# Kernel tuning notes

Measured on AMD Instinct MI355X. Metric: run time of the kernel, lower is better.

## Reference

```python
import jax, jax.numpy as jnp
import numpy as np

T, D, H, E, TOP_K = 4096, 512, 2048, 16, 2


def setup_inputs() -> dict:
    key = jax.random.key(0)
    ks = jax.random.split(key, 4)
    x = jax.random.normal(ks[0], (T, D), dtype=jnp.float32)
    Wg = jax.random.normal(ks[1], (D, E), dtype=jnp.float32) * 0.02
    bg = jnp.zeros((E,), dtype=jnp.float32)
    W1 = jax.random.normal(ks[2], (E, D, H), dtype=jnp.float32) * 0.02
    b1 = jnp.zeros((E, H), dtype=jnp.float32)
    W2 = jax.random.normal(ks[3], (E, H, D), dtype=jnp.float32) * 0.02
    b2 = jnp.zeros((E, D), dtype=jnp.float32)
    return {"x": x, "Wg": Wg, "bg": bg, "W1": W1, "b1": b1, "W2": W2, "b2": b2}


def reference(x, Wg, bg, W1, b1, W2, b2):
    # NaiveGate: linear -> top-k -> softmax over the k selected logits
    logits = x @ Wg + bg                               # [T, E]
    gate_vals, gate_idx = jax.lax.top_k(logits, TOP_K)  # [T, k]
    gate_score = jax.nn.softmax(gate_vals, axis=-1)     # returned by gate; NOT applied to output (faithful to source)

    # combine weights: how many top-k slots of each token map to each expert
    counts = jax.nn.one_hot(gate_idx, E, dtype=x.dtype).sum(axis=1)  # [T, E]

    # Expert FFN (grouped GEMM expressed densely over the fixed expert axis)
    h = jax.nn.gelu(jnp.einsum('td,edh->eth', x, W1) + b1[:, None, :])  # [E, T, H]
    y = jnp.einsum('eth,ehd->etd', h, W2) + b2[:, None, :]              # [E, T, D]

    # Combine: unweighted sum over the token's top-k experts (matches .sum(dim=1) in source)
    out = jnp.einsum('etd,te->td', y, counts)                            # [T, D]
    return out, gate_idx, gate_score
```

## Files before the change

### kernel.cpp

```cpp
#include <hip/hip_runtime.h>
#include <math.h>

#define T_ 4096
#define D_ 512
#define H_ 2048
#define E_ 16
#define RCAP 10240

typedef short bf16x8 __attribute__((ext_vector_type(8)));
typedef float f32x4 __attribute__((ext_vector_type(4)));

__device__ __forceinline__ unsigned short f2bf(float f) {
  union { float f; unsigned u; } v; v.f = f;
  unsigned r = v.u + 0x7fffu + ((v.u >> 16) & 1u);
  return (unsigned short)(r >> 16);
}
__device__ __forceinline__ float bf2f(unsigned short u) {
  union { unsigned u; float f; } v; v.u = ((unsigned)u) << 16;
  return v.f;
}

__global__ void gate_kernel(const float* __restrict__ x,
                            const float* __restrict__ Wg,
                            const float* __restrict__ bg,
                            float* __restrict__ out,
                            int* __restrict__ tok2e) {
  const int lane = threadIdx.x & 63;
  const int t = blockIdx.x * 4 + (threadIdx.x >> 6);
  const int e = lane & 15, q = lane >> 4;
  const float4* x4 = (const float4*)(x + (size_t)t * D_ + q * 128);
  float acc = 0.f;
#pragma unroll 4
  for (int i = 0; i < 32; ++i) {
    float4 v = x4[i];
    const float* wp = Wg + (q * 128 + i * 4) * E_ + e;
    acc += v.x * wp[0];
    acc += v.y * wp[E_];
    acc += v.z * wp[2 * E_];
    acc += v.w * wp[3 * E_];
  }
  acc += __shfl_xor(acc, 16);
  acc += __shfl_xor(acc, 32);
  const float logit = acc + bg[e];
  float v1 = logit; int i1 = e;
#pragma unroll
  for (int s = 1; s < 16; s <<= 1) {
    float ov = __shfl_xor(v1, s); int oi = __shfl_xor(i1, s);
    if (ov > v1 || (ov == v1 && oi < i1)) { v1 = ov; i1 = oi; }
  }
  float v2 = (e == i1) ? -INFINITY : logit; int i2 = e;
#pragma unroll
  for (int s = 1; s < 16; s <<= 1) {
    float ov = __shfl_xor(v2, s); int oi = __shfl_xor(i2, s);
    if (ov > v2 || (ov == v2 && oi < i2)) { v2 = ov; i2 = oi; }
  }
  if (lane == 0) {
    const float ed = __expf(v2 - v1);
    const float inv = 1.f / (1.f + ed);
    const size_t gidx = (size_t)T_ * D_;
    out[gidx + t * 2]     = (float)i1;
    out[gidx + t * 2 + 1] = (float)i2;
    out[gidx + T_ * 2 + t * 2]     = inv;
    out[gidx + T_ * 2 + t * 2 + 1] = ed * inv;
    tok2e[t * 2] = i1; tok2e[t * 2 + 1] = i2;
  }
}

__global__ void count_kernel(const int* __restrict__ tok2e,
                             int* __restrict__ cnt2,
                             int* __restrict__ offs, int* __restrict__ tileoff,
                             int* __restrict__ rowbuf) {
  __shared__ int h[E_];
  if (threadIdx.x < E_) h[threadIdx.x] = 0;
  __syncthreads();
  for (int i = threadIdx.x; i < 2 * T_; i += 256) atomicAdd(&h[tok2e[i]], 1);
  __syncthreads();
  if (threadIdx.x == 0) {
    int o = 0, to = 0;
    offs[0] = 0; tileoff[0] = 0;
    for (int e = 0; e < E_; ++e) {
      int mt = (h[e] + 127) >> 7;
      o += mt << 7; to += mt;
      offs[e + 1] = o; tileoff[e + 1] = to;
    }
  }
  for (int i = threadIdx.x; i < E_ * 16; i += 256) cnt2[i] = 0;
  for (int i = threadIdx.x; i < RCAP; i += 256) rowbuf[i] = -1;
}

__global__ void scatter_kernel(const int* __restrict__ tok2e, int* __restrict__ cnt2,
                               const int* __restrict__ offs, int* __restrict__ rowbuf,
                               int* __restrict__ tok2row) {
  const int t = blockIdx.x * blockDim.x + threadIdx.x;
#pragma unroll
  for (int k = 0; k < 2; ++k) {
    int e = tok2e[t * 2 + k];
    int slot = atomicAdd(&cnt2[e * 16], 1);
    int row = offs[e] + slot;
    rowbuf[row] = t;
    tok2row[t * 2 + k] = row;
  }
}

__global__ void gather_kernel(const float* __restrict__ x,
                              const int* __restrict__ rowbuf,
                              const int* __restrict__ offs,
                              unsigned short* __restrict__ xg) {
  const int row = blockIdx.x;
  if (row >= offs[16]) return;
  const int t = rowbuf[row];
  const int lane = threadIdx.x;
  float4 a = make_float4(0.f, 0.f, 0.f, 0.f), b = a;
  if (t >= 0) {
    const float4* p = (const float4*)(x + (size_t)t * D_ + lane * 8);
    a = p[0]; b = p[1];
  }
  unsigned w0 = f2bf(a.x) | (f2bf(a.y) << 16);
  unsigned w1 = f2bf(a.z) | (f2bf(a.w) << 16);
  unsigned w2 = f2bf(b.x) | (f2bf(b.y) << 16);
  unsigned w3 = f2bf(b.z) | (f2bf(b.w) << 16);
  *(uint4*)(xg + (size_t)row * D_ + lane * 8) = make_uint4(w0, w1, w2, w3);
}

template <int KDIM, int NTOT, bool GELU>
__global__ __launch_bounds__(256) void ffn_gemm(
    const unsigned short* __restrict__ A_g, const float* __restrict__ B_g,
    const float* __restrict__ bias_g, unsigned short* __restrict__ out_g,
    const int* __restrict__ offs, const int* __restrict__ tileoff) {
  __shared__ unsigned short As[128][72];
  __shared__ unsigned short Bs[128][72];
  const int mt = blockIdx.x;
  if (mt >= tileoff[16]) return;
  int e = 0;
  while (tileoff[e + 1] <= mt) ++e;
  const int row0 = offs[e] + ((mt - tileoff[e]) << 7);
  const int n0 = blockIdx.y << 7;
  const int tid = threadIdx.x;
  const int lane = tid & 63;
  const int m_off = ((tid >> 6) & 1) << 6;
  const int n_off = (tid >> 7) << 6;

  f32x4 zero = {0.f, 0.f, 0.f, 0.f};
  f32x4 acc[4][4];
#pragma unroll
  for (int i = 0; i < 4; ++i)
#pragma unroll
    for (int j = 0; j < 4; ++j) acc[i][j] = zero;

  const int arow = tid >> 1, ahalf = tid & 1;
  const unsigned short* Aptr = A_g + (size_t)(row0 + arow) * KDIM + ahalf * 32;
  const int bn = tid & 127, bkq = tid >> 7;
  const float* Bptr = B_g + (size_t)e * KDIM * NTOT + (size_t)(bkq * 32) * NTOT + n0 + bn;

  for (int k0 = 0; k0 < KDIM; k0 += 64) {
    const uint4* asrc = (const uint4*)(Aptr + k0);
    uint4 a0 = asrc[0], a1 = asrc[1], a2 = asrc[2], a3 = asrc[3];
    const float* bsrc = Bptr + (size_t)k0 * NTOT;
    unsigned w[16];
#pragma unroll
    for (int kk = 0; kk < 16; ++kk) {
      unsigned lo = f2bf(bsrc[(size_t)(2 * kk) * NTOT]);
      unsigned hi = f2bf(bsrc[(size_t)(2 * kk + 1) * NTOT]);
      w[kk] = lo | (hi << 16);
    }
    uint4* adst = (uint4*)&As[arow][ahalf * 32];
    adst[0] = a0; adst[1] = a1; adst[2] = a2; adst[3] = a3;
    uint4* bdst = (uint4*)&Bs[bn][bkq * 32];
    bdst[0] = make_uint4(w[0], w[1], w[2], w[3]);
    bdst[1] = make_uint4(w[4], w[5], w[6], w[7]);
    bdst[2] = make_uint4(w[8], w[9], w[10], w[11]);
    bdst[3] = make_uint4(w[12], w[13], w[14], w[15]);
    __syncthreads();
#pragma unroll
    for (int kk = 0; kk < 64; kk += 32) {
      const int kidx = kk + ((lane >> 4) << 3);
      bf16x8 af[4], bfr[4];
#pragma unroll
      for (int i = 0; i < 4; ++i)
        af[i] = *(const bf16x8*)&As[m_off + i * 16 + (lane & 15)][kidx];
#pragma unroll
      for (int j = 0; j < 4; ++j)
        bfr[j] = *(const bf16x8*)&Bs[n_off + j * 16 + (lane & 15)][kidx];
#pragma unroll
      for (int i = 0; i < 4; ++i)
#pragma unroll
        for (int j = 0; j < 4; ++j)
          acc[i][j] = __builtin_amdgcn_mfma_f32_16x16x32_bf16(af[i], bfr[j], acc[i][j], 0, 0, 0);
    }
    __syncthreads();
  }
  const float* bias = bias_g + (size_t)e * NTOT;
  const int quad = lane >> 4, lcol = lane & 15;
#pragma unroll
  for (int j = 0; j < 4; ++j) {
    const int col = n0 + n_off + j * 16 + lcol;
    const float bv = bias[col];
#pragma unroll
    for (int i = 0; i < 4; ++i) {
      const int rbase = row0 + m_off + i * 16 + (quad << 2);
      f32x4 v = acc[i][j];
#pragma unroll
      for (int r = 0; r < 4; ++r) {
        float y = v[r] + bv;
        if (GELU) y = 0.5f * y * (1.f + erff(y * 0.70710678118f));
        out_g[(size_t)(rbase + r) * NTOT + col] = f2bf(y);
      }
    }
  }
}

__global__ void combine_kernel(const unsigned short* __restrict__ ybuf,
                               const int* __restrict__ tok2row,
                               float* __restrict__ out) {
  const int t = blockIdx.x, lane = threadIdx.x;
  const int rA = tok2row[t * 2], rB = tok2row[t * 2 + 1];
  const uint4 va = *(const uint4*)(ybuf + (size_t)rA * D_ + lane * 8);
  const uint4 vb = *(const uint4*)(ybuf + (size_t)rB * D_ + lane * 8);
  const unsigned short* pa = (const unsigned short*)&va;
  const unsigned short* pb = (const unsigned short*)&vb;
  float o[8];
#pragma unroll
  for (int i = 0; i < 8; ++i) o[i] = bf2f(pa[i]) + bf2f(pb[i]);
  float4* po = (float4*)(out + (size_t)t * D_ + lane * 8);
  po[0] = make_float4(o[0], o[1], o[2], o[3]);
  po[1] = make_float4(o[4], o[5], o[6], o[7]);
}

extern "C" void kernel_launch(void* const* d_in, const int* in_sizes, int n_in,
                              void* d_out, int out_size, void* d_ws, size_t ws_size,
                              hipStream_t stream) {
  const float* x  = (const float*)d_in[0];
  const float* Wg = (const float*)d_in[1];
  const float* bg = (const float*)d_in[2];
  const float* W1 = (const float*)d_in[3];
  const float* b1 = (const float*)d_in[4];
  const float* W2 = (const float*)d_in[5];
  const float* b2 = (const float*)d_in[6];
  float* out = (float*)d_out;
  char* ws = (char*)d_ws;

  int* cnt2    = (int*)(ws);
  int* offs    = (int*)(ws + 2048);
  int* tileoff = (int*)(ws + 3072);
  int* tok2e   = (int*)(ws + 4096);
  int* tok2row = (int*)(ws + 4096 + 32768);
  int* rowbuf  = (int*)(ws + 4096 + 65536);
  unsigned short* xg   = (unsigned short*)(ws + (1 << 20));
  unsigned short* ybuf = xg;
  unsigned short* hbuf = (unsigned short*)(ws + (12 << 20));

  gate_kernel<<<T_ / 4, 256, 0, stream>>>(x, Wg, bg, out, tok2e);
  count_kernel<<<1, 256, 0, stream>>>(tok2e, cnt2, offs, tileoff, rowbuf);
  scatter_kernel<<<T_ / 256, 256, 0, stream>>>(tok2e, cnt2, offs, rowbuf, tok2row);
  gather_kernel<<<RCAP, 64, 0, stream>>>(x, rowbuf, offs, xg);
  ffn_gemm<512, 2048, true><<<dim3(80, 16), 256, 0, stream>>>(xg, W1, b1, hbuf, offs, tileoff);
  ffn_gemm<2048, 512, false><<<dim3(80, 4), 256, 0, stream>>>(hbuf, W2, b2, ybuf, offs, tileoff);
  combine_kernel<<<T_, 64, 0, stream>>>(ybuf, tok2row, out);
}
```

Before: 341.7 us.

## Pre-transpose expert weights to bf16 K-major and shrink second GEMM N-tile

Adds a transpose kernel that converts each expert weight matrix from fp32 [K,N] to bf16 [N,K] before each GEMM. The GEMM then loads B tiles with contiguous 16-byte vector loads instead of strided scalar fp32 loads followed by in-loop conversion. The second GEMM also moves to a 64-wide N tile, which doubles its grid in y to expose more parallelism. The cost is an extra pass over the weights on every call, about 64MB of fp32 read and 32MB of bf16 written per matrix, plus more workspace.

```diff
diff --git a/kernel.cpp b/kernel.cpp
--- a/kernel.cpp
+++ b/kernel.cpp
@@ -122,69 +122,92 @@
   *(uint4*)(xg + (size_t)row * D_ + lane * 8) = make_uint4(w0, w1, w2, w3);
 }
 
-template <int KDIM, int NTOT, bool GELU>
+template <int K, int N>
+__global__ __launch_bounds__(256) void wtrans_kernel(const float* __restrict__ src,
+                                                     unsigned short* __restrict__ dst) {
+  __shared__ unsigned short tile[64][72];
+  const int e = blockIdx.z;
+  const int n0 = blockIdx.x << 6, k0 = blockIdx.y << 6;
+  const int tid = threadIdx.x;
+  const int tr = tid >> 4, tc = (tid & 15) << 2;
+  const float* s = src + ((size_t)e * K + k0) * N + n0;
+#pragma unroll
+  for (int p = 0; p < 4; ++p) {
+    float4 v = *(const float4*)(s + (size_t)(tr + p * 16) * N + tc);
+    tile[tc + 0][tr + p * 16] = f2bf(v.x);
+    tile[tc + 1][tr + p * 16] = f2bf(v.y);
+    tile[tc + 2][tr + p * 16] = f2bf(v.z);
+    tile[tc + 3][tr + p * 16] = f2bf(v.w);
+  }
+  __syncthreads();
+  const int wr = tid >> 2, wc = (tid & 3) << 4;
+  unsigned short* d = dst + ((size_t)e * N + n0 + wr) * K + k0 + wc;
+  *(uint4*)d       = *(const uint4*)&tile[wr][wc];
+  *(uint4*)(d + 8) = *(const uint4*)&tile[wr][wc + 8];
+}
+
+template <int KDIM, int NTOT, int NTILE, bool GELU>
 __global__ __launch_bounds__(256) void ffn_gemm(
-    const unsigned short* __restrict__ A_g, const float* __restrict__ B_g,
+    const unsigned short* __restrict__ A_g, const unsigned short* __restrict__ Bt_g,
     const float* __restrict__ bias_g, unsigned short* __restrict__ out_g,
     const int* __restrict__ offs, const int* __restrict__ tileoff) {
+  constexpr int JN = NTILE / 32;
   __shared__ unsigned short As[128][72];
-  __shared__ unsigned short Bs[128][72];
+  __shared__ unsigned short Bs[NTILE][72];
   const int mt = blockIdx.x;
   if (mt >= tileoff[16]) return;
   int e = 0;
   while (tileoff[e + 1] <= mt) ++e;
   const int row0 = offs[e] + ((mt - tileoff[e]) << 7);
-  const int n0 = blockIdx.y << 7;
+  const int n0 = blockIdx.y * NTILE;
   const int tid = threadIdx.x;
   const int lane = tid & 63;
   const int m_off = ((tid >> 6) & 1) << 6;
-  const int n_off = (tid >> 7) << 6;
-
-  f32x4 zero = {0.f, 0.f, 0.f, 0.f};
-  f32x4 acc[4][4];
+  const int n_off = (tid >> 7) * (NTILE / 2);
+
+  f32x4 acc[4][JN];
 #pragma unroll
   for (int i = 0; i < 4; ++i)
 #pragma unroll
-    for (int j = 0; j < 4; ++j) acc[i][j] = zero;
+    for (int j = 0; j < JN; ++j) acc[i][j] = (f32x4){0.f, 0.f, 0.f, 0.f};
 
   const int arow = tid >> 1, ahalf = tid & 1;
   const unsigned short* Aptr = A_g + (size_t)(row0 + arow) * KDIM + ahalf * 32;
-  const int bn = tid & 127, bkq = tid >> 7;
-  const float* Bptr = B_g + (size_t)e * KDIM * NTOT + (size_t)(bkq * 32) * NTOT + n0 + bn;
+  int brow, bcol;
+  if (NTILE == 128) { brow = tid >> 1; bcol = (tid & 1) * 32; }
+  else              { brow = tid >> 2; bcol = (tid & 3) * 16; }
+  const unsigned short* Bptr = Bt_g + ((size_t)e * NTOT + n0 + brow) * KDIM + bcol;
 
   for (int k0 = 0; k0 < KDIM; k0 += 64) {
     const uint4* asrc = (const uint4*)(Aptr + k0);
     uint4 a0 = asrc[0], a1 = asrc[1], a2 = asrc[2], a3 = asrc[3];
-    const float* bsrc = Bptr + (size_t)k0 * NTOT;
-    unsigned w[16];
-#pragma unroll
-    for (int kk = 0; kk < 16; ++kk) {
-      unsigned lo = f2bf(bsrc[(size_t)(2 * kk) * NTOT]);
-      unsigned hi = f2bf(bsrc[(size_t)(2 * kk + 1) * NTOT]);
-      w[kk] = lo | (hi << 16);
-    }
+    const uint4* bsrc = (const uint4*)(Bptr + k0);
+    uint4 b0 = bsrc[0], b1 = bsrc[1], b2, b3;
+    if (NTILE == 128) { b2 = bsrc[2]; b3 = bsrc[3]; }
     uint4* adst = (uint4*)&As[arow][ahalf * 32];
     adst[0] = a0; adst[1] = a1; adst[2] = a2; adst[3] = a3;
-    uint4* bdst = (uint4*)&Bs[bn][bkq * 32];
-    bdst[0] = make_uint4(w[0], w[1], w[2], w[3]);
-    bdst[1] = make_uint4(w[4], w[5], w[6], w[7]);
-    bdst[2] = make_uint4(w[8], w[9], w[10], w[11]);
-    bdst[3] = make_uint4(w[12], w[13], w[14], w[15]);
+    if (NTILE == 128) {
+      uint4* bdst = (uint4*)&Bs[brow][bcol];
+      bdst[0] = b0; bdst[1] = b1; bdst[2] = b2; bdst[3] = b3;
+    } else {
+      uint4* bdst = (uint4*)&Bs[brow][bcol];
+      bdst[0] = b0; bdst[1] = b1;
+    }
     __syncthreads();
 #pragma unroll
     for (int kk = 0; kk < 64; kk += 32) {
       const int kidx = kk + ((lane >> 4) << 3);
-      bf16x8 af[4], bfr[4];
+      bf16x8 af[4], bfr[JN];
 #pragma unroll
       for (int i = 0; i < 4; ++i)
         af[i] = *(const bf16x8*)&As[m_off + i * 16 + (lane & 15)][kidx];
 #pragma unroll
-      for (int j = 0; j < 4; ++j)
+      for (int j = 0; j < JN; ++j)
         bfr[j] = *(const bf16x8*)&Bs[n_off + j * 16 + (lane & 15)][kidx];
 #pragma unroll
       for (int i = 0; i < 4; ++i)
 #pragma unroll
-        for (int j = 0; j < 4; ++j)
+        for (int j = 0; j < JN; ++j)
           acc[i][j] = __builtin_amdgcn_mfma_f32_16x16x32_bf16(af[i], bfr[j], acc[i][j], 0, 0, 0);
     }
     __syncthreads();
@@ -192,7 +215,7 @@
   const float* bias = bias_g + (size_t)e * NTOT;
   const int quad = lane >> 4, lcol = lane & 15;
 #pragma unroll
-  for (int j = 0; j < 4; ++j) {
+  for (int j = 0; j < JN; ++j) {
     const int col = n0 + n_off + j * 16 + lcol;
     const float bv = bias[col];
 #pragma unroll
@@ -247,13 +270,16 @@
   int* rowbuf  = (int*)(ws + 4096 + 65536);
   unsigned short* xg   = (unsigned short*)(ws + (1 << 20));
   unsigned short* ybuf = xg;
-  unsigned short* hbuf = (unsigned short*)(ws + (12 << 20));
+  unsigned short* hbuf = (unsigned short*)(ws + (size_t)(12 << 20));
+  unsigned short* Wt   = (unsigned short*)(ws + (size_t)(52 << 20));
 
   gate_kernel<<<T_ / 4, 256, 0, stream>>>(x, Wg, bg, out, tok2e);
   count_kernel<<<1, 256, 0, stream>>>(tok2e, cnt2, offs, tileoff, rowbuf);
   scatter_kernel<<<T_ / 256, 256, 0, stream>>>(tok2e, cnt2, offs, rowbuf, tok2row);
   gather_kernel<<<RCAP, 64, 0, stream>>>(x, rowbuf, offs, xg);
-  ffn_gemm<512, 2048, true><<<dim3(80, 16), 256, 0, stream>>>(xg, W1, b1, hbuf, offs, tileoff);
-  ffn_gemm<2048, 512, false><<<dim3(80, 4), 256, 0, stream>>>(hbuf, W2, b2, ybuf, offs, tileoff);
+  wtrans_kernel<D_, H_><<<dim3(H_ / 64, D_ / 64, E_), 256, 0, stream>>>(W1, Wt);
+  ffn_gemm<512, 2048, 128, true><<<dim3(80, 16), 256, 0, stream>>>(xg, Wt, b1, hbuf, offs, tileoff);
+  wtrans_kernel<H_, D_><<<dim3(D_ / 64, H_ / 64, E_), 256, 0, stream>>>(W2, Wt);
+  ffn_gemm<2048, 512, 64, false><<<dim3(80, 8), 256, 0, stream>>>(hbuf, Wt, b2, ybuf, offs, tileoff);
   combine_kernel<<<T_, 64, 0, stream>>>(ybuf, tok2row, out);
 }
```

Measured after the change: 315.5 us. 7.6% less time.
